# Kernel optimization log

Hardware: AMD Instinct MI355X
Metric: run time of the kernel (lower is better)

The kernel has to match this reference:

```python
import jax, jax.numpy as jnp
import numpy as np

ACT_BW = 8
PAR_BW = 4
EPS = 1e-8

def fake_quant(t, bw):
    # symmetric per-tensor fake quantization with dynamic absmax observer
    qmax = float(2 ** (bw - 1) - 1)
    scale = jnp.maximum(jnp.max(jnp.abs(t)) / qmax, EPS)
    q = jnp.clip(jnp.round(t / scale), -qmax, qmax) * scale
    # straight-through estimator (matches torch fake-quant backward)
    return t + jax.lax.stop_gradient(q - t)

def setup_inputs() -> dict:
    key = jax.random.key(0)
    k1, k2, k3 = jax.random.split(key, 3)
    tokens, d_in, d_out = 4096, 4096, 4096
    x = jax.random.normal(k1, (tokens, d_in), dtype=jnp.float32)
    # kaiming-uniform-ish init scale
    bound_w = 1.0 / np.sqrt(d_in)
    weight = jax.random.uniform(k2, (d_out, d_in), dtype=jnp.float32, minval=-bound_w, maxval=bound_w)
    b = jax.random.uniform(k3, (d_out,), dtype=jnp.float32, minval=-bound_w, maxval=bound_w)
    return {"x": x, "weight": weight, "b": b}

def reference(x, weight, b):
    # 1) requantize input activations (act_bitwidth)
    xq = fake_quant(x, ACT_BW)
    # 2) quantize weight (par_bitwidth), transpose [out,in] -> [in,out]
    wq = fake_quant(weight, PAR_BW).T
    # 3) quantize bias (act_bitwidth)
    bq = fake_quant(b, ACT_BW)
    # 4) AddMM: bias + x @ w^T, then requantize the output (multiplier's quantizer)
    out = bq + jnp.matmul(xq, wq)  # [tokens, out_features]
    return fake_quant(out, ACT_BW)
```

## Files before the change

kernel.cpp:

```cpp
#include <hip/hip_runtime.h>

#define NELEM (4096 * 4096)
#define KDIM 4096
#define NDIM 4096
#define DOUT 4096
#define EPSQ 1e-8f

typedef __attribute__((ext_vector_type(4))) int i32x4;

typedef __attribute__((address_space(3))) void lds_void;
typedef const __attribute__((address_space(1))) void gbl_void;

__device__ __forceinline__ void load_lds16(const void* g, void* l) {
    __builtin_amdgcn_global_load_lds((gbl_void*)g, (lds_void*)l, 16, 0, 0);
}

__device__ __forceinline__ float wave_max64(float v) {
#pragma unroll
    for (int off = 32; off > 0; off >>= 1)
        v = fmaxf(v, __shfl_down(v, off));
    return v;
}

__global__ void zero_ws(unsigned* __restrict__ amax) {
    if (threadIdx.x < 4) amax[threadIdx.x] = 0u;
}

__global__ __launch_bounds__(256) void absmax_xwb(
    const float4* __restrict__ x, const float4* __restrict__ w,
    const float* __restrict__ b, unsigned* __restrict__ amax)
{
    const int n4 = NELEM / 4;
    float mx = 0.f, mw = 0.f;
    for (int i = blockIdx.x * 256 + threadIdx.x; i < n4; i += gridDim.x * 256) {
        float4 a = x[i];
        mx = fmaxf(mx, fmaxf(fmaxf(fabsf(a.x), fabsf(a.y)), fmaxf(fabsf(a.z), fabsf(a.w))));
        float4 c = w[i];
        mw = fmaxf(mw, fmaxf(fmaxf(fabsf(c.x), fabsf(c.y)), fmaxf(fabsf(c.z), fabsf(c.w))));
    }
    float mb = 0.f;
    if (blockIdx.x == 0)
        for (int i = threadIdx.x; i < DOUT; i += 256) mb = fmaxf(mb, fabsf(b[i]));

    mx = wave_max64(mx); mw = wave_max64(mw); mb = wave_max64(mb);
    __shared__ float red[3][4];
    const int wave = threadIdx.x >> 6, lane = threadIdx.x & 63;
    if (lane == 0) { red[0][wave] = mx; red[1][wave] = mw; red[2][wave] = mb; }
    __syncthreads();
    if (threadIdx.x == 0) {
        float r0 = fmaxf(fmaxf(red[0][0], red[0][1]), fmaxf(red[0][2], red[0][3]));
        float r1 = fmaxf(fmaxf(red[1][0], red[1][1]), fmaxf(red[1][2], red[1][3]));
        atomicMax(&amax[0], __float_as_uint(r0));
        atomicMax(&amax[1], __float_as_uint(r1));
        if (blockIdx.x == 0) {
            float r2 = fmaxf(fmaxf(red[2][0], red[2][1]), fmaxf(red[2][2], red[2][3]));
            atomicMax(&amax[2], __float_as_uint(r2));
        }
    }
}

__device__ __forceinline__ int pack4(float4 a, float s, float qmax) {
    int b0 = (int)fminf(fmaxf(rintf(a.x / s), -qmax), qmax);
    int b1 = (int)fminf(fmaxf(rintf(a.y / s), -qmax), qmax);
    int b2 = (int)fminf(fmaxf(rintf(a.z / s), -qmax), qmax);
    int b3 = (int)fminf(fmaxf(rintf(a.w / s), -qmax), qmax);
    return (b0 & 0xff) | ((b1 & 0xff) << 8) | ((b2 & 0xff) << 16) | (b3 << 24);
}

__global__ __launch_bounds__(256) void quant_xwb(
    const float4* __restrict__ x, const float4* __restrict__ w,
    const float* __restrict__ b, const unsigned* __restrict__ amax,
    int4* __restrict__ qx, int4* __restrict__ qw, float* __restrict__ bq)
{
    const float sx = fmaxf(__uint_as_float(amax[0]) / 127.0f, EPSQ);
    const float sw = fmaxf(__uint_as_float(amax[1]) / 7.0f, EPSQ);
    const int n16 = NELEM / 16;
    for (int i = blockIdx.x * 256 + threadIdx.x; i < n16; i += gridDim.x * 256) {
        int4 r;
        r.x = pack4(x[i * 4 + 0], sx, 127.f);
        r.y = pack4(x[i * 4 + 1], sx, 127.f);
        r.z = pack4(x[i * 4 + 2], sx, 127.f);
        r.w = pack4(x[i * 4 + 3], sx, 127.f);
        qx[i] = r;
        int4 p;
        p.x = pack4(w[i * 4 + 0], sw, 7.f);
        p.y = pack4(w[i * 4 + 1], sw, 7.f);
        p.z = pack4(w[i * 4 + 2], sw, 7.f);
        p.w = pack4(w[i * 4 + 3], sw, 7.f);
        qw[i] = p;
    }
    if (blockIdx.x == 0) {
        const float sb = fmaxf(__uint_as_float(amax[2]) / 127.0f, EPSQ);
        for (int i = threadIdx.x; i < DOUT; i += 256) {
            float q = fminf(fmaxf(rintf(b[i] / sb), -127.f), 127.f);
            bq[i] = q * sb;
        }
    }
}

__global__ __launch_bounds__(256, 2) void gemm_i8(
    const char* __restrict__ qx,
    const char* __restrict__ qw,
    const float* __restrict__ bq,
    const unsigned* __restrict__ amax,
    float* __restrict__ out,
    unsigned* __restrict__ amax_out)
{
    constexpr int K = KDIM, N = NDIM, BK = 64;
    __shared__ char smemA[128 * BK];
    __shared__ char smemB[128 * BK];
    __shared__ float red[4];

    const int tid = threadIdx.x;
    const int wave = tid >> 6;
    const int lane = tid & 63;
    const int bm = blockIdx.y, bn = blockIdx.x;

    const int wm = (wave & 1) * 64;
    const int wn = (wave >> 1) * 64;

    i32x4 acc[4][4] = {};

    const int srow = wave * 16 + (lane >> 2);
    const int scol = (lane & 3) * 16;
    const char* aP0 = qx + (long)(bm * 128 + srow) * K + scol;
    const char* aP1 = aP0 + 64 * K;
    const char* bP0 = qw + (long)(bn * 128 + srow) * K + scol;
    const char* bP1 = bP0 + 64 * K;
    char* aL0 = smemA + wave * 1024;
    char* aL1 = aL0 + 4096;
    char* bL0 = smemB + wave * 1024;
    char* bL1 = bL0 + 4096;

    const int frow = lane & 15;
    const int fk = (lane >> 4) * 16;

    for (int k0 = 0; k0 < K; k0 += BK) {
        __syncthreads();
        load_lds16(aP0 + k0, aL0);
        load_lds16(aP1 + k0, aL1);
        load_lds16(bP0 + k0, bL0);
        load_lds16(bP1 + k0, bL1);
        __syncthreads();

        i32x4 af[4], bf[4];
#pragma unroll
        for (int i = 0; i < 4; ++i)
            af[i] = *(const i32x4*)(smemA + (wm + i * 16 + frow) * BK + fk);
#pragma unroll
        for (int j = 0; j < 4; ++j)
            bf[j] = *(const i32x4*)(smemB + (wn + j * 16 + frow) * BK + fk);
#pragma unroll
        for (int i = 0; i < 4; ++i)
#pragma unroll
            for (int j = 0; j < 4; ++j)
                acc[i][j] = __builtin_amdgcn_mfma_i32_16x16x64_i8(af[i], bf[j], acc[i][j], 0, 0, 0);
    }

    const float sx = fmaxf(__uint_as_float(amax[0]) / 127.0f, EPSQ);
    const float sw = fmaxf(__uint_as_float(amax[1]) / 7.0f, EPSQ);
    const float s = sx * sw;
    const int col = lane & 15;
    const int rbase = (lane >> 4) * 4;
    float am = 0.f;
    float bqv[4];
#pragma unroll
    for (int j = 0; j < 4; ++j) bqv[j] = bq[bn * 128 + wn + j * 16 + col];

#pragma unroll
    for (int i = 0; i < 4; ++i) {
#pragma unroll
        for (int r = 0; r < 4; ++r) {
            const int m = bm * 128 + wm + i * 16 + rbase + r;
            float* orow = out + (long)m * N + bn * 128 + wn + col;
#pragma unroll
            for (int j = 0; j < 4; ++j) {
                float o = fmaf(s, (float)acc[i][j][r], bqv[j]);
                am = fmaxf(am, fabsf(o));
                orow[j * 16] = o;
            }
        }
    }
    am = wave_max64(am);
    if (lane == 0) red[wave] = am;
    __syncthreads();
    if (tid == 0)
        atomicMax(amax_out, __float_as_uint(fmaxf(fmaxf(red[0], red[1]), fmaxf(red[2], red[3]))));
}

__global__ __launch_bounds__(256) void final_quant(
    float4* __restrict__ out, const unsigned* __restrict__ amax)
{
    const float so = fmaxf(__uint_as_float(amax[3]) / 127.0f, EPSQ);
    const int n4 = NELEM / 4;
    for (int i = blockIdx.x * 256 + threadIdx.x; i < n4; i += gridDim.x * 256) {
        float4 v = out[i];
        v.x = fminf(fmaxf(rintf(v.x / so), -127.f), 127.f) * so;
        v.y = fminf(fmaxf(rintf(v.y / so), -127.f), 127.f) * so;
        v.z = fminf(fmaxf(rintf(v.z / so), -127.f), 127.f) * so;
        v.w = fminf(fmaxf(rintf(v.w / so), -127.f), 127.f) * so;
        out[i] = v;
    }
}

extern "C" void kernel_launch(void* const* d_in, const int* in_sizes, int n_in,
                              void* d_out, int out_size, void* d_ws, size_t ws_size,
                              hipStream_t stream) {
    const float* x = (const float*)d_in[0];
    const float* w = (const float*)d_in[1];
    const float* b = (const float*)d_in[2];
    float* out = (float*)d_out;

    char* ws = (char*)d_ws;
    unsigned* amax = (unsigned*)ws;
    float* bq = (float*)(ws + 256);
    char* qx = (char*)(ws + 32768);
    char* qw = (char*)(ws + 32768 + (size_t)NELEM);

    hipLaunchKernelGGL(zero_ws, dim3(1), dim3(64), 0, stream, amax);
    hipLaunchKernelGGL(absmax_xwb, dim3(2048), dim3(256), 0, stream,
                       (const float4*)x, (const float4*)w, b, amax);
    hipLaunchKernelGGL(quant_xwb, dim3(2048), dim3(256), 0, stream,
                       (const float4*)x, (const float4*)w, b, amax,
                       (int4*)qx, (int4*)qw, bq);
    hipLaunchKernelGGL(gemm_i8, dim3(32, 32), dim3(256), 0, stream,
                       qx, qw, bq, amax, out, amax + 3);
    hipLaunchKernelGGL(final_quant, dim3(2048), dim3(256), 0, stream,
                       (float4*)out, amax);
}
```

Baseline: 319.1 us.

## Swizzle GEMM LDS layout, unroll fixed-trip elementwise loops, memset workspace

```diff
diff --git a/kernel.cpp b/kernel.cpp
--- a/kernel.cpp
+++ b/kernel.cpp
@@ -5,6 +5,7 @@
 #define NDIM 4096
 #define DOUT 4096
 #define EPSQ 1e-8f
+#define STRIDE_MEM (2048 * 256)
 
 typedef __attribute__((ext_vector_type(4))) int i32x4;
 
@@ -22,25 +23,25 @@
     return v;
 }
 
-__global__ void zero_ws(unsigned* __restrict__ amax) {
-    if (threadIdx.x < 4) amax[threadIdx.x] = 0u;
-}
-
 __global__ __launch_bounds__(256) void absmax_xwb(
     const float4* __restrict__ x, const float4* __restrict__ w,
     const float* __restrict__ b, unsigned* __restrict__ amax)
 {
-    const int n4 = NELEM / 4;
     float mx = 0.f, mw = 0.f;
-    for (int i = blockIdx.x * 256 + threadIdx.x; i < n4; i += gridDim.x * 256) {
+    int i = blockIdx.x * 256 + threadIdx.x;
+#pragma unroll
+    for (int it = 0; it < 8; ++it, i += STRIDE_MEM) {
         float4 a = x[i];
+        float4 c = w[i];
         mx = fmaxf(mx, fmaxf(fmaxf(fabsf(a.x), fabsf(a.y)), fmaxf(fabsf(a.z), fabsf(a.w))));
-        float4 c = w[i];
         mw = fmaxf(mw, fmaxf(fmaxf(fabsf(c.x), fabsf(c.y)), fmaxf(fabsf(c.z), fabsf(c.w))));
     }
     float mb = 0.f;
-    if (blockIdx.x == 0)
-        for (int i = threadIdx.x; i < DOUT; i += 256) mb = fmaxf(mb, fabsf(b[i]));
+    if (blockIdx.x == 0) {
+#pragma unroll
+        for (int t = 0; t < DOUT / 256; ++t)
+            mb = fmaxf(mb, fabsf(b[t * 256 + threadIdx.x]));
+    }
 
     mx = wave_max64(mx); mw = wave_max64(mw); mb = wave_max64(mb);
     __shared__ float red[3][4];
@@ -74,8 +75,9 @@
 {
     const float sx = fmaxf(__uint_as_float(amax[0]) / 127.0f, EPSQ);
     const float sw = fmaxf(__uint_as_float(amax[1]) / 7.0f, EPSQ);
-    const int n16 = NELEM / 16;
-    for (int i = blockIdx.x * 256 + threadIdx.x; i < n16; i += gridDim.x * 256) {
+    int i = blockIdx.x * 256 + threadIdx.x;
+#pragma unroll
+    for (int it = 0; it < 2; ++it, i += STRIDE_MEM) {
         int4 r;
         r.x = pack4(x[i * 4 + 0], sx, 127.f);
         r.y = pack4(x[i * 4 + 1], sx, 127.f);
@@ -91,9 +93,11 @@
     }
     if (blockIdx.x == 0) {
         const float sb = fmaxf(__uint_as_float(amax[2]) / 127.0f, EPSQ);
-        for (int i = threadIdx.x; i < DOUT; i += 256) {
-            float q = fminf(fmaxf(rintf(b[i] / sb), -127.f), 127.f);
-            bq[i] = q * sb;
+#pragma unroll
+        for (int t = 0; t < DOUT / 256; ++t) {
+            int j = t * 256 + threadIdx.x;
+            float q = fminf(fmaxf(rintf(b[j] / sb), -127.f), 127.f);
+            bq[j] = q * sb;
         }
     }
 }
@@ -122,7 +126,7 @@
     i32x4 acc[4][4] = {};
 
     const int srow = wave * 16 + (lane >> 2);
-    const int scol = (lane & 3) * 16;
+    const int scol = (((lane & 3) ^ ((lane >> 3) & 3)) << 4);
     const char* aP0 = qx + (long)(bm * 128 + srow) * K + scol;
     const char* aP1 = aP0 + 64 * K;
     const char* bP0 = qw + (long)(bn * 128 + srow) * K + scol;
@@ -133,7 +137,7 @@
     char* bL1 = bL0 + 4096;
 
     const int frow = lane & 15;
-    const int fk = (lane >> 4) * 16;
+    const int fks = (((lane >> 4) ^ ((frow >> 1) & 3)) << 4);
 
     for (int k0 = 0; k0 < K; k0 += BK) {
         __syncthreads();
@@ -146,10 +150,10 @@
         i32x4 af[4], bf[4];
 #pragma unroll
         for (int i = 0; i < 4; ++i)
-            af[i] = *(const i32x4*)(smemA + (wm + i * 16 + frow) * BK + fk);
+            af[i] = *(const i32x4*)(smemA + (wm + i * 16 + frow) * BK + fks);
 #pragma unroll
         for (int j = 0; j < 4; ++j)
-            bf[j] = *(const i32x4*)(smemB + (wn + j * 16 + frow) * BK + fk);
+            bf[j] = *(const i32x4*)(smemB + (wn + j * 16 + frow) * BK + fks);
 #pragma unroll
         for (int i = 0; i < 4; ++i)
 #pragma unroll
@@ -192,8 +196,9 @@
     float4* __restrict__ out, const unsigned* __restrict__ amax)
 {
     const float so = fmaxf(__uint_as_float(amax[3]) / 127.0f, EPSQ);
-    const int n4 = NELEM / 4;
-    for (int i = blockIdx.x * 256 + threadIdx.x; i < n4; i += gridDim.x * 256) {
+    int i = blockIdx.x * 256 + threadIdx.x;
+#pragma unroll
+    for (int it = 0; it < 8; ++it, i += STRIDE_MEM) {
         float4 v = out[i];
         v.x = fminf(fmaxf(rintf(v.x / so), -127.f), 127.f) * so;
         v.y = fminf(fmaxf(rintf(v.y / so), -127.f), 127.f) * so;
@@ -217,7 +222,7 @@
     char* qx = (char*)(ws + 32768);
     char* qw = (char*)(ws + 32768 + (size_t)NELEM);
 
-    hipLaunchKernelGGL(zero_ws, dim3(1), dim3(64), 0, stream, amax);
+    hipMemsetAsync(amax, 0, 16, stream);
     hipLaunchKernelGGL(absmax_xwb, dim3(2048), dim3(256), 0, stream,
                        (const float4*)x, (const float4*)w, b, amax);
     hipLaunchKernelGGL(quant_xwb, dim3(2048), dim3(256), 0, stream,
```

Result: faster. 300.4 us (-5.9%).
